# Kernel optimization log

Hardware: AMD Instinct MI355X
Metric: run time of the kernel (lower is better)

The kernel has to match this reference:

```python
import jax, jax.numpy as jnp
import numpy as np

D_MODEL = 1024
NUM_HEADS = 16
HEAD_DIM = D_MODEL // NUM_HEADS
B, S = 4, 2048


def setup_inputs() -> dict:
    key = jax.random.key(0)
    ks = jax.random.split(key, 11)
    scale = 1.0 / np.sqrt(D_MODEL)
    inp = {
        "query": jax.random.normal(ks[0], (B, S, D_MODEL), dtype=jnp.float32),
        "key": jax.random.normal(ks[1], (B, S, D_MODEL), dtype=jnp.float32),
        "value": jax.random.normal(ks[2], (B, S, D_MODEL), dtype=jnp.float32),
        "Wq": jax.random.normal(ks[3], (D_MODEL, D_MODEL), dtype=jnp.float32) * scale,
        "bq": jnp.zeros((D_MODEL,), dtype=jnp.float32),
        "Wk": jax.random.normal(ks[4], (D_MODEL, D_MODEL), dtype=jnp.float32) * scale,
        "bk": jnp.zeros((D_MODEL,), dtype=jnp.float32),
        "Wv": jax.random.normal(ks[5], (D_MODEL, D_MODEL), dtype=jnp.float32) * scale,
        "bv": jnp.zeros((D_MODEL,), dtype=jnp.float32),
        "Wo": jax.random.normal(ks[6], (D_MODEL, D_MODEL), dtype=jnp.float32) * scale,
        "bo": jnpp.zeros((D_MODEL,), dtype=jnp.float32) if False else jnp.zeros((D_MODEL,), dtype=jnp.float32),
    }
    return inp


def reference(query, key, value, Wq, bq, Wk, bk, Wv, bv, Wo, bo):
    # Linear projections (torch Linear: x @ W.T + b), split into heads: [B,H,S,Dh]
    def split_heads(x):
        b, s, _ = x.shape
        return x.reshape(b, s, NUM_HEADS, HEAD_DIM).transpose(0, 2, 1, 3)

    q = split_heads(query @ Wq.T + bq)
    k = split_heads(key @ Wk.T + bk)
    v = split_heads(value @ Wv.T + bv)

    # Explicit attention: [B,H,S,S] scores, softmax, AV
    scores = jnp.einsum("bhqd,bhkd->bhqk", q, k) / np.sqrt(HEAD_DIM).astype(np.float32)
    attn = jax.nn.softmax(scores, axis=-1)
    ctx = jnp.einsum("bhqk,bhkd->bhqd", attn, v)

    # Merge heads and output projection
    b = ctx.shape[0]
    ctx = ctx.transpose(0, 2, 1, 3).reshape(b, -1, D_MODEL)
    return ctx @ Wo.T + bo
```

## Files before the change

### kernel.cpp

```cpp
#include <hip/hip_runtime.h>
#include <stdint.h>

#define DMODEL 1024
#define NHEADS 16
#define HDIM   64
#define BB     4
#define SS     2048
#define MM     (BB*SS)
#define QKV_ELEMS ((size_t)8388608)

typedef unsigned short ushort_t;
typedef __bf16    bf16x8  __attribute__((ext_vector_type(8)));
typedef _Float16  half4   __attribute__((ext_vector_type(4)));
typedef _Float16  half2_t __attribute__((ext_vector_type(2)));
typedef float     floatx4 __attribute__((ext_vector_type(4)));

__device__ inline ushort_t f32_to_bf16(float f) {
    union { float f; uint32_t u; } v; v.f = f;
    uint32_t r = v.u + 0x7FFF + ((v.u >> 16) & 1);
    return (ushort_t)(r >> 16);
}
__device__ inline ushort_t f32_to_f16u(float f) {
    union { _Float16 h; ushort_t u; } v; v.h = (_Float16)f; return v.u;
}
__device__ inline half2_t pkrtz(float a, float b) {
    return __builtin_bit_cast(half2_t, __builtin_amdgcn_cvt_pkrtz(a, b));
}
__device__ inline void glds16(const void* g, void* l) {
    __builtin_amdgcn_global_load_lds(
        (const __attribute__((address_space(1))) unsigned int*)g,
        (__attribute__((address_space(3))) unsigned int*)l, 16, 0, 0);
}

__global__ __launch_bounds__(256) void convert_bf16(const float* __restrict__ in,
                                                    ushort_t* __restrict__ out) {
    size_t i = ((size_t)blockIdx.x * 256 + threadIdx.x) * 8;
    float4 a = *(const float4*)&in[i];
    float4 b = *(const float4*)&in[i + 4];
    ushort_t t[8];
    t[0] = f32_to_bf16(a.x); t[1] = f32_to_bf16(a.y);
    t[2] = f32_to_bf16(a.z); t[3] = f32_to_bf16(a.w);
    t[4] = f32_to_bf16(b.x); t[5] = f32_to_bf16(b.y);
    t[6] = f32_to_bf16(b.z); t[7] = f32_to_bf16(b.w);
    *(uint4*)&out[i] = *(uint4*)t;
}

__global__ __launch_bounds__(256) void convert_w3(
    const float* __restrict__ w0, const float* __restrict__ w1, const float* __restrict__ w2,
    ushort_t* __restrict__ o0, ushort_t* __restrict__ o1, ushort_t* __restrict__ o2) {
    const float* src = (blockIdx.y == 0) ? w0 : (blockIdx.y == 1) ? w1 : w2;
    ushort_t*    dst = (blockIdx.y == 0) ? o0 : (blockIdx.y == 1) ? o1 : o2;
    size_t i = ((size_t)blockIdx.x * 256 + threadIdx.x) * 8;
    float4 a = *(const float4*)&src[i];
    float4 b = *(const float4*)&src[i + 4];
    ushort_t t[8];
    t[0] = f32_to_bf16(a.x); t[1] = f32_to_bf16(a.y);
    t[2] = f32_to_bf16(a.z); t[3] = f32_to_bf16(a.w);
    t[4] = f32_to_bf16(b.x); t[5] = f32_to_bf16(b.y);
    t[6] = f32_to_bf16(b.z); t[7] = f32_to_bf16(b.w);
    *(uint4*)&dst[i] = *(uint4*)t;
}

template<int OUT>
__global__ __launch_bounds__(256) void gemm_bf16(
    const ushort_t* __restrict__ A, const ushort_t* __restrict__ W,
    const float* __restrict__ bias, void* __restrict__ O, float scale)
{
    __shared__ ushort_t As[2 * 128 * 32];
    __shared__ ushort_t Bs[2 * 128 * 32];

    const int tid  = threadIdx.x;
    const int lane = tid & 63;
    const int quad = lane >> 4;
    const int l15  = lane & 15;
    const int wid  = tid >> 6;
    const int wr   = wid >> 1, wc = wid & 1;
    const int m0   = blockIdx.y * 128;
    const int n0   = blockIdx.x * 128;

    floatx4 acc[4][4];
    #pragma unroll
    for (int i = 0; i < 4; i++)
        #pragma unroll
        for (int j = 0; j < 4; j++)
            acc[i][j] = (floatx4){0.f, 0.f, 0.f, 0.f};

    #pragma unroll
    for (int j = 0; j < 2; j++) {
        const int p = tid + j * 256, row = p >> 2, cc = p & 3;
        glds16(&A[(size_t)(m0 + row) * DMODEL + cc * 8], &As[p * 8]);
        glds16(&W[(size_t)(n0 + row) * DMODEL + cc * 8], &Bs[p * 8]);
    }

    for (int k0 = 0; k0 < DMODEL; k0 += 32) {
        const int cb = ((k0 >> 5) & 1) * (128 * 32);
        const int nbo = (128 * 32) - cb;
        __syncthreads();
        const int kn = (k0 + 32) & (DMODEL - 1);
        #pragma unroll
        for (int j = 0; j < 2; j++) {
            const int p = tid + j * 256, row = p >> 2, cc = p & 3;
            glds16(&A[(size_t)(m0 + row) * DMODEL + kn + cc * 8], &As[nbo + p * 8]);
            glds16(&W[(size_t)(n0 + row) * DMODEL + kn + cc * 8], &Bs[nbo + p * 8]);
        }
        bf16x8 af[4], bf[4];
        #pragma unroll
        for (int i = 0; i < 4; i++)
            af[i] = *(const bf16x8*)&As[cb + (wr * 64 + i * 16 + l15) * 32 + quad * 8];
        #pragma unroll
        for (int j = 0; j < 4; j++)
            bf[j] = *(const bf16x8*)&Bs[cb + (wc * 64 + j * 16 + l15) * 32 + quad * 8];
        #pragma unroll
        for (int i = 0; i < 4; i++)
            #pragma unroll
            for (int j = 0; j < 4; j++)
                acc[i][j] = __builtin_amdgcn_mfma_f32_16x16x32_bf16(af[i], bf[j], acc[i][j], 0, 0, 0);
    }

    #pragma unroll
    for (int j = 0; j < 4; j++) {
        const int n = n0 + wc * 64 + j * 16 + l15;
        const float bn = bias[n];
        #pragma unroll
        for (int i = 0; i < 4; i++) {
            #pragma unroll
            for (int r = 0; r < 4; r++) {
                const int m = m0 + wr * 64 + i * 16 + quad * 4 + r;
                float v = (acc[i][j][r] + bn) * scale;
                if (OUT == 0) {
                    const int b = m >> 11, s = m & 2047;
                    const int hh = n >> 6, dh = n & 63;
                    ((ushort_t*)O)[(((size_t)(b * NHEADS + hh)) * SS + s) * HDIM + dh] = f32_to_bf16(v);
                } else if (OUT == 1) {
                    const int b = m >> 11, s = m & 2047;
                    const int hh = n >> 6, dh = n & 63;
                    ((ushort_t*)O)[(((size_t)(b * NHEADS + hh)) * SS + s) * HDIM + dh] = f32_to_f16u(v);
                } else {
                    ((float*)O)[(size_t)m * DMODEL + n] = v;
                }
            }
        }
    }
}

__global__ __launch_bounds__(256, 4) void attn_kernel(
    const ushort_t* __restrict__ Q, const ushort_t* __restrict__ K,
    const ushort_t* __restrict__ V, ushort_t* __restrict__ ctx)
{
    constexpr int LDV = 72;
    constexpr int VOFF = 2 * 4096;
    __shared__ ushort_t smem[2 * 4096 + 2 * 64 * LDV];
    ushort_t* Tr = smem;

    const int tid  = threadIdx.x;
    const int lane = tid & 63;
    const int wid  = tid >> 6;
    const int quad = lane >> 4;
    const int l15  = lane & 15;
    const int bid  = blockIdx.x;
    const int bh   = (bid & 7) * 8 + (bid >> 7);
    const int b    = bh >> 4, h = bh & 15;
    const int q0   = ((bid >> 3) & 15) * 128 + wid * 32;

    const ushort_t* Qb = Q + (size_t)bh * SS * HDIM;
    const ushort_t* Kb = K + (size_t)bh * SS * HDIM;
    const ushort_t* Vb = V + (size_t)bh * SS * HDIM;

    bf16x8 qf[2][2];
    #pragma unroll
    for (int qt = 0; qt < 2; qt++)
        #pragma unroll
        for (int c = 0; c < 2; c++)
            qf[qt][c] = *(const bf16x8*)&Qb[(size_t)(q0 + qt * 16 + l15) * HDIM + c * 32 + quad * 8];

    floatx4 acc[2][4];
    #pragma unroll
    for (int qt = 0; qt < 2; qt++)
        #pragma unroll
        for (int dt = 0; dt < 4; dt++)
            acc[qt][dt] = (floatx4){0.f, 0.f, 0.f, 0.f};
    float mrun[2] = {-1e30f, -1e30f};
    float lrun[2] = {0.f, 0.f};

    const int kp = tid & 31;
    const int dc = tid >> 5;

    #pragma unroll
    for (int j = 0; j < 2; j++) {
        const int p = tid + j * 256, row = p >> 3, cc = (p & 7) ^ (row & 7);
        glds16(&Kb[(size_t)row * HDIM + cc * 8], &smem[p * 8]);
    }
    {
        ushort_t ua[8], ub[8];
        *(uint4*)ua = *(const uint4*)&Vb[(size_t)(2 * kp) * HDIM + dc * 8];
        *(uint4*)ub = *(const uint4*)&Vb[(size_t)(2 * kp + 1) * HDIM + dc * 8];
        #pragma unroll
        for (int i = 0; i < 8; i++)
            *(uint32_t*)&smem[VOFF + (dc * 8 + i) * LDV + 2 * kp] = (uint32_t)ua[i] | ((uint32_t)ub[i] << 16);
    }

    const half2_t one2 = {(_Float16)1.f, (_Float16)1.f};

    for (int kt = 0; kt < SS; kt += 64) {
        const int cur = ((kt >> 6) & 1);
        const int ko  = cur * 4096;
        const int kon = 4096 - ko;
        const int vo  = VOFF + cur * (64 * LDV);
        const int von = VOFF + (64 * LDV) - cur * (64 * LDV);
        __syncthreads();

        const int ktn = (kt + 64) & (SS - 1);
        #pragma unroll
        for (int j = 0; j < 2; j++) {
            const int p = tid + j * 256, row = p >> 3, cc = (p & 7) ^ (row & 7);
            glds16(&Kb[(size_t)(ktn + row) * HDIM + cc * 8], &smem[kon + p * 8]);
        }
        ushort_t ua[8], ub[8];
        *(uint4*)ua = *(const uint4*)&Vb[(size_t)(ktn + 2 * kp) * HDIM + dc * 8];
        *(uint4*)ub = *(const uint4*)&Vb[(size_t)(ktn + 2 * kp + 1) * HDIM + dc * 8];

        bf16x8 kf[4][2];
        #pragma unroll
        for (int nt = 0; nt < 4; nt++) {
            const int row = nt * 16 + l15;
            #pragma unroll
            for (int c = 0; c < 2; c++) {
                const int pos = (c * 4 + quad) ^ (row & 7);
                kf[nt][c] = *(const bf16x8*)&smem[ko + row * 64 + pos * 8];
            }
        }
        half4 vf[4][4];
        #pragma unroll
        for (int kb = 0; kb < 4; kb++)
            #pragma unroll
            for (int dt = 0; dt < 4; dt++)
                vf[kb][dt] = *(const half4*)&smem[vo + (dt * 16 + l15) * LDV + kb * 16 + quad * 4];

        #pragma unroll
        for (int qt = 0; qt < 2; qt++) {
            floatx4 s[4];
            #pragma unroll
            for (int nt = 0; nt < 4; nt++) {
                floatx4 cz = (floatx4){0.f, 0.f, 0.f, 0.f};
                cz = __builtin_amdgcn_mfma_f32_16x16x32_bf16(kf[nt][0], qf[qt][0], cz, 0, 0, 0);
                cz = __builtin_amdgcn_mfma_f32_16x16x32_bf16(kf[nt][1], qf[qt][1], cz, 0, 0, 0);
                s[nt] = cz;
            }
            float mx = s[0][0];
            #pragma unroll
            for (int nt = 0; nt < 4; nt++)
                #pragma unroll
                for (int r = 0; r < 4; r++) mx = fmaxf(mx, s[nt][r]);
            mx = fmaxf(mx, __shfl_xor(mx, 16));
            mx = fmaxf(mx, __shfl_xor(mx, 32));
            const float mnew  = fmaxf(mrun[qt], mx);
            const float alpha = __builtin_amdgcn_exp2f(mrun[qt] - mnew);
            mrun[qt] = mnew;

            float ps = 0.f;
            half4 pf[4];
            #pragma unroll
            for (int nt = 0; nt < 4; nt++) {
                const float p0 = __builtin_amdgcn_exp2f(s[nt][0] - mnew);
                const float p1 = __builtin_amdgcn_exp2f(s[nt][1] - mnew);
                const float p2 = __builtin_amdgcn_exp2f(s[nt][2] - mnew);
                const float p3 = __builtin_amdgcn_exp2f(s[nt][3] - mnew);
                const half2_t ha = pkrtz(p0, p1);
                const half2_t hb = pkrtz(p2, p3);
                ps = __builtin_amdgcn_fdot2(ha, one2, ps, false);
                ps = __builtin_amdgcn_fdot2(hb, one2, ps, false);
                union { half4 h4; half2_t h2[2]; } u;
                u.h2[0] = ha; u.h2[1] = hb;
                pf[nt] = u.h4;
            }
            ps += __shfl_xor(ps, 16);
            ps += __shfl_xor(ps, 32);
            lrun[qt] = lrun[qt] * alpha + ps;

            #pragma unroll
            for (int dt = 0; dt < 4; dt++) acc[qt][dt] *= alpha;
            #pragma unroll
            for (int kb = 0; kb < 4; kb++)
                #pragma unroll
                for (int dt = 0; dt < 4; dt++)
                    acc[qt][dt] = __builtin_amdgcn_mfma_f32_16x16x16f16(vf[kb][dt], pf[kb], acc[qt][dt], 0, 0, 0);
        }

        #pragma unroll
        for (int i = 0; i < 8; i++)
            *(uint32_t*)&smem[von + (dc * 8 + i) * LDV + 2 * kp] = (uint32_t)ua[i] | ((uint32_t)ub[i] << 16);
    }

    __syncthreads();
    const float inv0 = 1.f / lrun[0], inv1 = 1.f / lrun[1];
    ushort_t* Tw = Tr + wid * (32 * LDV);
    #pragma unroll
    for (int qt = 0; qt < 2; qt++) {
        const float inv = qt ? inv1 : inv0;
        #pragma unroll
        for (int dt = 0; dt < 4; dt++)
            #pragma unroll
            for (int r = 0; r < 4; r++)
                Tw[(qt * 16 + l15) * LDV + dt * 16 + quad * 4 + r] = f32_to_bf16(acc[qt][dt][r] * inv);
    }
    const int row = lane >> 1, hf = lane & 1;
    const ushort_t* src = Tw + row * LDV + hf * 32;
    ushort_t* dst = ctx + ((size_t)(b * SS) + q0 + row) * DMODEL + h * HDIM + hf * 32;
    #pragma unroll
    for (int i = 0; i < 4; i++)
        *(uint4*)(dst + i * 8) = *(const uint4*)(src + i * 8);
}

extern "C" void kernel_launch(void* const* d_in, const int* in_sizes, int n_in,
                              void* d_out, int out_size, void* d_ws, size_t ws_size,
                              hipStream_t stream) {
    (void)in_sizes; (void)n_in; (void)out_size; (void)ws_size;
    const float* query = (const float*)d_in[0];
    const float* key_  = (const float*)d_in[1];
    const float* value = (const float*)d_in[2];
    const float* Wq = (const float*)d_in[3];
    const float* bq = (const float*)d_in[4];
    const float* Wk = (const float*)d_in[5];
    const float* bk = (const float*)d_in[6];
    const float* Wv = (const float*)d_in[7];
    const float* bv = (const float*)d_in[8];
    const float* Wo = (const float*)d_in[9];
    const float* bo = (const float*)d_in[10];
    float* out = (float*)d_out;

    ushort_t* tmp = (ushort_t*)d_ws;
    ushort_t* Qw  = tmp + QKV_ELEMS;
    ushort_t* Kw  = Qw + QKV_ELEMS;
    ushort_t* Vw  = Kw + QKV_ELEMS;
    ushort_t* ctx = tmp;
    ushort_t* Wqb = (ushort_t*)d_out;
    ushort_t* Wkb = Wqb + 1048576;
    ushort_t* Wvb = Wkb + 1048576;
    ushort_t* Wob = Qw;

    dim3 blk(256);
    dim3 gg(DMODEL / 128, MM / 128);

    hipLaunchKernelGGL(convert_w3, dim3(512, 3), blk, 0, stream, Wq, Wk, Wv, Wqb, Wkb, Wvb);

    hipLaunchKernelGGL(convert_bf16, dim3(4096), blk, 0, stream, query, tmp);
    hipLaunchKernelGGL((gemm_bf16<0>), gg, blk, 0, stream, tmp, Wqb, bq, (void*)Qw, 0.18033688011f);
    hipLaunchKernelGGL(convert_bf16, dim3(4096), blk, 0, stream, key_, tmp);
    hipLaunchKernelGGL((gemm_bf16<0>), gg, blk, 0, stream, tmp, Wkb, bk, (void*)Kw, 1.0f);
    hipLaunchKernelGGL(convert_bf16, dim3(4096), blk, 0, stream, value, tmp);
    hipLaunchKernelGGL((gemm_bf16<1>), gg, blk, 0, stream, tmp, Wvb, bv, (void*)Vw, 1.0f);

    hipLaunchKernelGGL(attn_kernel, dim3(1024), blk, 0, stream, Qw, Kw, Vw, ctx);

    hipLaunchKernelGGL(convert_bf16, dim3(512), blk, 0, stream, Wo, Wob);
    hipLaunchKernelGGL((gemm_bf16<2>), gg, blk, 0, stream, ctx, Wob, bo, (void*)out, 1.0f);
}
```

Before: 404.8 us.

## Write V transposed from projection and async-load it in attention; batch Q/K GEMMs

The V projection epilogue now writes f16 V in a head-major transposed [B,H,Dh,S] layout as 4-wide vector stores. The attention kernel can then stream V tiles into LDS with async global_load_lds and XOR swizzling, replacing the per-iteration register transpose and scalar LDS writes. The Q and K input conversions and projections are merged into single launches to cut launch count and raise occupancy. The transposed V stores stride by S across d, which may make writes less coalesced, and an extra barrier is added before the context write-out.

```diff
diff --git a/kernel.cpp b/kernel.cpp
--- a/kernel.cpp
+++ b/kernel.cpp
@@ -19,9 +19,6 @@
     union { float f; uint32_t u; } v; v.f = f;
     uint32_t r = v.u + 0x7FFF + ((v.u >> 16) & 1);
     return (ushort_t)(r >> 16);
-}
-__device__ inline ushort_t f32_to_f16u(float f) {
-    union { _Float16 h; ushort_t u; } v; v.h = (_Float16)f; return v.u;
 }
 __device__ inline half2_t pkrtz(float a, float b) {
     return __builtin_bit_cast(half2_t, __builtin_amdgcn_cvt_pkrtz(a, b));
@@ -43,6 +40,22 @@
     t[4] = f32_to_bf16(b.x); t[5] = f32_to_bf16(b.y);
     t[6] = f32_to_bf16(b.z); t[7] = f32_to_bf16(b.w);
     *(uint4*)&out[i] = *(uint4*)t;
+}
+
+__global__ __launch_bounds__(256) void convert_a2(
+    const float* __restrict__ s0, const float* __restrict__ s1,
+    ushort_t* __restrict__ d0, ushort_t* __restrict__ d1) {
+    const float* src = blockIdx.y ? s1 : s0;
+    ushort_t*    dst = blockIdx.y ? d1 : d0;
+    size_t i = ((size_t)blockIdx.x * 256 + threadIdx.x) * 8;
+    float4 a = *(const float4*)&src[i];
+    float4 b = *(const float4*)&src[i + 4];
+    ushort_t t[8];
+    t[0] = f32_to_bf16(a.x); t[1] = f32_to_bf16(a.y);
+    t[2] = f32_to_bf16(a.z); t[3] = f32_to_bf16(a.w);
+    t[4] = f32_to_bf16(b.x); t[5] = f32_to_bf16(b.y);
+    t[6] = f32_to_bf16(b.z); t[7] = f32_to_bf16(b.w);
+    *(uint4*)&dst[i] = *(uint4*)t;
 }
 
 __global__ __launch_bounds__(256) void convert_w3(
@@ -62,21 +75,18 @@
 }
 
 template<int OUT>
-__global__ __launch_bounds__(256) void gemm_bf16(
+__device__ __forceinline__ void gemm_core(
+    ushort_t* As, ushort_t* Bs,
     const ushort_t* __restrict__ A, const ushort_t* __restrict__ W,
-    const float* __restrict__ bias, void* __restrict__ O, float scale)
-{
-    __shared__ ushort_t As[2 * 128 * 32];
-    __shared__ ushort_t Bs[2 * 128 * 32];
-
+    const float* __restrict__ bias, void* __restrict__ O, float scale,
+    int m0, int n0)
+{
     const int tid  = threadIdx.x;
     const int lane = tid & 63;
     const int quad = lane >> 4;
     const int l15  = lane & 15;
     const int wid  = tid >> 6;
     const int wr   = wid >> 1, wc = wid & 1;
-    const int m0   = blockIdx.y * 128;
-    const int n0   = blockIdx.x * 128;
 
     floatx4 acc[4][4];
     #pragma unroll
@@ -93,7 +103,7 @@
     }
 
     for (int k0 = 0; k0 < DMODEL; k0 += 32) {
-        const int cb = ((k0 >> 5) & 1) * (128 * 32);
+        const int cb  = ((k0 >> 5) & 1) * (128 * 32);
         const int nbo = (128 * 32) - cb;
         __syncthreads();
         const int kn = (k0 + 32) & (DMODEL - 1);
@@ -121,35 +131,78 @@
     for (int j = 0; j < 4; j++) {
         const int n = n0 + wc * 64 + j * 16 + l15;
         const float bn = bias[n];
-        #pragma unroll
-        for (int i = 0; i < 4; i++) {
-            #pragma unroll
-            for (int r = 0; r < 4; r++) {
-                const int m = m0 + wr * 64 + i * 16 + quad * 4 + r;
-                float v = (acc[i][j][r] + bn) * scale;
-                if (OUT == 0) {
-                    const int b = m >> 11, s = m & 2047;
-                    const int hh = n >> 6, dh = n & 63;
-                    ((ushort_t*)O)[(((size_t)(b * NHEADS + hh)) * SS + s) * HDIM + dh] = f32_to_bf16(v);
-                } else if (OUT == 1) {
-                    const int b = m >> 11, s = m & 2047;
-                    const int hh = n >> 6, dh = n & 63;
-                    ((ushort_t*)O)[(((size_t)(b * NHEADS + hh)) * SS + s) * HDIM + dh] = f32_to_f16u(v);
-                } else {
-                    ((float*)O)[(size_t)m * DMODEL + n] = v;
+        if (OUT == 1) {
+            const int hh = n >> 6, dh = n & 63;
+            #pragma unroll
+            for (int i = 0; i < 4; i++) {
+                const int m = m0 + wr * 64 + i * 16 + quad * 4;
+                const int b = m >> 11, s = m & 2047;
+                half4 hv;
+                #pragma unroll
+                for (int r = 0; r < 4; r++) hv[r] = (_Float16)(acc[i][j][r] + bn);
+                *(half4*)&((ushort_t*)O)[(((size_t)(b * NHEADS + hh)) * HDIM + dh) * SS + s] = hv;
+            }
+        } else {
+            #pragma unroll
+            for (int i = 0; i < 4; i++) {
+                #pragma unroll
+                for (int r = 0; r < 4; r++) {
+                    const int m = m0 + wr * 64 + i * 16 + quad * 4 + r;
+                    float v = (acc[i][j][r] + bn) * scale;
+                    if (OUT == 0) {
+                        const int b = m >> 11, s = m & 2047;
+                        const int hh = n >> 6, dh = n & 63;
+                        ((ushort_t*)O)[(((size_t)(b * NHEADS + hh)) * SS + s) * HDIM + dh] = f32_to_bf16(v);
+                    } else {
+                        ((float*)O)[(size_t)m * DMODEL + n] = v;
+                    }
                 }
             }
         }
     }
+}
+
+__global__ __launch_bounds__(256) void gemm_qk(
+    const ushort_t* __restrict__ qa, const ushort_t* __restrict__ ka,
+    const ushort_t* __restrict__ Wq, const ushort_t* __restrict__ Wk,
+    const float* __restrict__ bq, const float* __restrict__ bk,
+    ushort_t* __restrict__ Qo, ushort_t* __restrict__ Ko, float qscale)
+{
+    __shared__ ushort_t As[2 * 128 * 32];
+    __shared__ ushort_t Bs[2 * 128 * 32];
+    const int seg = blockIdx.x >> 3;
+    const int n0  = (blockIdx.x & 7) * 128;
+    const int m0  = blockIdx.y * 128;
+    if (seg == 0)
+        gemm_core<0>(As, Bs, qa, Wq, bq, (void*)Qo, qscale, m0, n0);
+    else
+        gemm_core<0>(As, Bs, ka, Wk, bk, (void*)Ko, 1.0f, m0, n0);
+}
+
+__global__ __launch_bounds__(256) void gemm_v(
+    const ushort_t* __restrict__ A, const ushort_t* __restrict__ W,
+    const float* __restrict__ bias, ushort_t* __restrict__ O)
+{
+    __shared__ ushort_t As[2 * 128 * 32];
+    __shared__ ushort_t Bs[2 * 128 * 32];
+    gemm_core<1>(As, Bs, A, W, bias, (void*)O, 1.0f, blockIdx.y * 128, blockIdx.x * 128);
+}
+
+__global__ __launch_bounds__(256) void gemm_o(
+    const ushort_t* __restrict__ A, const ushort_t* __restrict__ W,
+    const float* __restrict__ bias, float* __restrict__ O)
+{
+    __shared__ ushort_t As[2 * 128 * 32];
+    __shared__ ushort_t Bs[2 * 128 * 32];
+    gemm_core<2>(As, Bs, A, W, bias, (void*)O, 1.0f, blockIdx.y * 128, blockIdx.x * 128);
 }
 
 __global__ __launch_bounds__(256, 4) void attn_kernel(
     const ushort_t* __restrict__ Q, const ushort_t* __restrict__ K,
-    const ushort_t* __restrict__ V, ushort_t* __restrict__ ctx)
-{
-    constexpr int LDV = 72;
+    const ushort_t* __restrict__ VT, ushort_t* __restrict__ ctx)
+{
     constexpr int VOFF = 2 * 4096;
-    __shared__ ushort_t smem[2 * 4096 + 2 * 64 * LDV];
+    __shared__ ushort_t smem[4 * 4096];
     ushort_t* Tr = smem;
 
     const int tid  = threadIdx.x;
@@ -162,9 +215,9 @@
     const int b    = bh >> 4, h = bh & 15;
     const int q0   = ((bid >> 3) & 15) * 128 + wid * 32;
 
-    const ushort_t* Qb = Q + (size_t)bh * SS * HDIM;
-    const ushort_t* Kb = K + (size_t)bh * SS * HDIM;
-    const ushort_t* Vb = V + (size_t)bh * SS * HDIM;
+    const ushort_t* Qb = Q  + (size_t)bh * SS * HDIM;
+    const ushort_t* Kb = K  + (size_t)bh * SS * HDIM;
+    const ushort_t* Vb = VT + (size_t)bh * HDIM * SS;
 
     bf16x8 qf[2][2];
     #pragma unroll
@@ -182,21 +235,11 @@
     float mrun[2] = {-1e30f, -1e30f};
     float lrun[2] = {0.f, 0.f};
 
-    const int kp = tid & 31;
-    const int dc = tid >> 5;
-
     #pragma unroll
     for (int j = 0; j < 2; j++) {
         const int p = tid + j * 256, row = p >> 3, cc = (p & 7) ^ (row & 7);
         glds16(&Kb[(size_t)row * HDIM + cc * 8], &smem[p * 8]);
-    }
-    {
-        ushort_t ua[8], ub[8];
-        *(uint4*)ua = *(const uint4*)&Vb[(size_t)(2 * kp) * HDIM + dc * 8];
-        *(uint4*)ub = *(const uint4*)&Vb[(size_t)(2 * kp + 1) * HDIM + dc * 8];
-        #pragma unroll
-        for (int i = 0; i < 8; i++)
-            *(uint32_t*)&smem[VOFF + (dc * 8 + i) * LDV + 2 * kp] = (uint32_t)ua[i] | ((uint32_t)ub[i] << 16);
+        glds16(&Vb[(size_t)row * SS + cc * 8], &smem[VOFF + p * 8]);
     }
 
     const half2_t one2 = {(_Float16)1.f, (_Float16)1.f};
@@ -205,8 +248,6 @@
         const int cur = ((kt >> 6) & 1);
         const int ko  = cur * 4096;
         const int kon = 4096 - ko;
-        const int vo  = VOFF + cur * (64 * LDV);
-        const int von = VOFF + (64 * LDV) - cur * (64 * LDV);
         __syncthreads();
 
         const int ktn = (kt + 64) & (SS - 1);
@@ -214,10 +255,8 @@
         for (int j = 0; j < 2; j++) {
             const int p = tid + j * 256, row = p >> 3, cc = (p & 7) ^ (row & 7);
             glds16(&Kb[(size_t)(ktn + row) * HDIM + cc * 8], &smem[kon + p * 8]);
-        }
-        ushort_t ua[8], ub[8];
-        *(uint4*)ua = *(const uint4*)&Vb[(size_t)(ktn + 2 * kp) * HDIM + dc * 8];
-        *(uint4*)ub = *(const uint4*)&Vb[(size_t)(ktn + 2 * kp + 1) * HDIM + dc * 8];
+            glds16(&Vb[(size_t)row * SS + ktn + cc * 8], &smem[VOFF + kon + p * 8]);
+        }
 
         bf16x8 kf[4][2];
         #pragma unroll
@@ -231,10 +270,15 @@
         }
         half4 vf[4][4];
         #pragma unroll
-        for (int kb = 0; kb < 4; kb++)
-            #pragma unroll
-            for (int dt = 0; dt < 4; dt++)
-                vf[kb][dt] = *(const half4*)&smem[vo + (dt * 16 + l15) * LDV + kb * 16 + quad * 4];
+        for (int kb = 0; kb < 4; kb++) {
+            #pragma unroll
+            for (int dt = 0; dt < 4; dt++) {
+                const int row = dt * 16 + l15;
+                const int u   = kb * 4 + quad;
+                const int g   = (u >> 1) ^ (row & 7);
+                vf[kb][dt] = *(const half4*)&smem[VOFF + ko + row * 64 + g * 8 + (u & 1) * 4];
+            }
+        }
 
         #pragma unroll
         for (int qt = 0; qt < 2; qt++) {
@@ -285,15 +329,12 @@
                 for (int dt = 0; dt < 4; dt++)
                     acc[qt][dt] = __builtin_amdgcn_mfma_f32_16x16x16f16(vf[kb][dt], pf[kb], acc[qt][dt], 0, 0, 0);
         }
-
-        #pragma unroll
-        for (int i = 0; i < 8; i++)
-            *(uint32_t*)&smem[von + (dc * 8 + i) * LDV + 2 * kp] = (uint32_t)ua[i] | ((uint32_t)ub[i] << 16);
     }
 
     __syncthreads();
+    constexpr int LDT = 72;
     const float inv0 = 1.f / lrun[0], inv1 = 1.f / lrun[1];
-    ushort_t* Tw = Tr + wid * (32 * LDV);
+    ushort_t* Tw = Tr + wid * (32 * LDT);
     #pragma unroll
     for (int qt = 0; qt < 2; qt++) {
         const float inv = qt ? inv1 : inv0;
@@ -301,10 +342,11 @@
         for (int dt = 0; dt < 4; dt++)
             #pragma unroll
             for (int r = 0; r < 4; r++)
-                Tw[(qt * 16 + l15) * LDV + dt * 16 + quad * 4 + r] = f32_to_bf16(acc[qt][dt][r] * inv);
-    }
+                Tw[(qt * 16 + l15) * LDT + dt * 16 + quad * 4 + r] = f32_to_bf16(acc[qt][dt][r] * inv);
+    }
+    __syncthreads();
     const int row = lane >> 1, hf = lane & 1;
-    const ushort_t* src = Tw + row * LDV + hf * 32;
+    const ushort_t* src = Tw + row * LDT + hf * 32;
     ushort_t* dst = ctx + ((size_t)(b * SS) + q0 + row) * DMODEL + h * HDIM + hf * 32;
     #pragma unroll
     for (int i = 0; i < 4; i++)
@@ -328,30 +370,27 @@
     const float* bo = (const float*)d_in[10];
     float* out = (float*)d_out;
 
-    ushort_t* tmp = (ushort_t*)d_ws;
-    ushort_t* Qw  = tmp + QKV_ELEMS;
-    ushort_t* Kw  = Qw + QKV_ELEMS;
-    ushort_t* Vw  = Kw + QKV_ELEMS;
-    ushort_t* ctx = tmp;
+    ushort_t* t1 = (ushort_t*)d_ws;
+    ushort_t* t2 = t1 + QKV_ELEMS;
+    ushort_t* t3 = t2 + QKV_ELEMS;
+    ushort_t* t4 = t3 + QKV_ELEMS;
     ushort_t* Wqb = (ushort_t*)d_out;
     ushort_t* Wkb = Wqb + 1048576;
     ushort_t* Wvb = Wkb + 1048576;
-    ushort_t* Wob = Qw;
 
     dim3 blk(256);
-    dim3 gg(DMODEL / 128, MM / 128);
 
     hipLaunchKernelGGL(convert_w3, dim3(512, 3), blk, 0, stream, Wq, Wk, Wv, Wqb, Wkb, Wvb);
-
-    hipLaunchKernelGGL(convert_bf16, dim3(4096), blk, 0, stream, query, tmp);
-    hipLaunchKernelGGL((gemm_bf16<0>), gg, blk, 0, stream, tmp, Wqb, bq, (void*)Qw, 0.18033688011f);
-    hipLaunchKernelGGL(convert_bf16, dim3(4096), blk, 0, stream, key_, tmp);
-    hipLaunchKernelGGL((gemm_bf16<0>), gg, blk, 0, stream, tmp, Wkb, bk, (void*)Kw, 1.0f);
-    hipLaunchKernelGGL(convert_bf16, dim3(4096), blk, 0, stream, value, tmp);
-    hipLaunchKernelGGL((gemm_bf16<1>), gg, blk, 0, stream, tmp, Wvb, bv, (void*)Vw, 1.0f);
-
-    hipLaunchKernelGGL(attn_kernel, dim3(1024), blk, 0, stream, Qw, Kw, Vw, ctx);
-
-    hipLaunchKernelGGL(convert_bf16, dim3(512), blk, 0, stream, Wo, Wob);
-    hipLaunchKernelGGL((gemm_bf16<2>), gg, blk, 0, stream, ctx, Wob, bo, (void*)out, 1.0f);
-}
+    hipLaunchKernelGGL(convert_a2, dim3(4096, 2), blk, 0, stream, query, key_, t1, t2);
+
+    hipLaunchKernelGGL(gemm_qk, dim3(16, 64), blk, 0, stream,
+                       t1, t2, Wqb, Wkb, bq, bk, t3, t4, 0.18033688011f);
+
+    hipLaunchKernelGGL(convert_bf16, dim3(4096), blk, 0, stream, value, t1);
+    hipLaunchKernelGGL(gemm_v, dim3(8, 64), blk, 0, stream, t1, Wvb, bv, t2);
+
+    hipLaunchKernelGGL(attn_kernel, dim3(1024), blk, 0, stream, t3, t4, t2, t1);
+
+    hipLaunchKernelGGL(convert_bf16, dim3(512), blk, 0, stream, Wo, t3);
+    hipLaunchKernelGGL(gemm_o, dim3(8, 64), blk, 0, stream, t1, t3, bo, out);
+}
```

Result: no change. 412.2 us (+1.8%).
